# Optimization experiments

Measured on AMD Instinct MI355X. Metric: run time of the kernel, lower is better.

## Reference

```python
import jax, jax.numpy as jnp
import numpy as np

G = 16          # horizontal stripes
K = 4           # latents per stripe
TEMP = 0.125
TOPK_RATIO = 0.125
GATE_THR = 0.05
EPS = 1e-6
KSZ = 3


def setup_inputs() -> dict:
    key = jax.random.key(0)
    k1, k2 = jax.random.split(key)
    x = jax.random.normal(k1, (64, 256, 64, 44), dtype=jnp.float32)
    latent_basis = jax.random.normal(k2, (G, K, 256), dtype=jnp.float32)
    return {"x": x, "latent_basis": latent_basis}


def _avg_pool3(x):
    # x: [n, g, c, sh, w]; 3x3 avg pool, stride 1, pad 1, count_include_pad=True
    s = jax.lax.reduce_window(x, 0.0, jax.lax.add,
                              (1, 1, 1, KSZ, KSZ), (1, 1, 1, 1, 1),
                              [(0, 0), (0, 0), (0, 0), (1, 1), (1, 1)])
    return s / float(KSZ * KSZ)


def _l2norm(v, axis=-1):
    return v / jnp.maximum(jnp.linalg.norm(v, axis=axis, keepdims=True), 1e-12)


def reference(x, latent_basis):
    n, c, h, w = x.shape
    sh = h // G
    p = sh * w
    # split into horizontal stripes: [n, g, c, sh, w]
    xr = x.reshape(n, c, G, sh, w).transpose(0, 2, 1, 3, 4)
    support_feat = _avg_pool3(xr)
    feat_flat = xr.transpose(0, 1, 3, 4, 2).reshape(n, G, p, c)          # ngpc
    support_flat = support_feat.transpose(0, 1, 3, 4, 2).reshape(n, G, p, c)

    # active mask from detached feature energy
    e = jax.lax.stop_gradient(xr).astype(jnp.float32)
    fe = jnp.mean(e * e, axis=2)                                          # n g sh w
    fe = fe / jnp.maximum(jnp.max(fe, axis=(-2, -1), keepdims=True), EPS)
    active = (fe > GATE_THR).astype(jnp.float32)
    fallback = (fe > 0).astype(jnp.float32)
    use_fb = jnp.sum(active, axis=(-2, -1), keepdims=True) <= 0
    active = jnp.where(use_fb, fallback, active).reshape(n, G, p)

    # cosine-similarity routing
    sfn = _l2norm(support_flat)
    lbn = _l2norm(latent_basis)                                           # g k c
    logits = jnp.einsum('ngpc,gkc->ngpk', sfn, lbn) / TEMP
    route_prob = jax.nn.softmax(logits, axis=-1)
    support = route_prob * active[..., None]                              # n g p k
    pool_w = support / jnp.maximum(jnp.sum(support, axis=2, keepdims=True), EPS)
    tokens = jnp.einsum('ngpk,ngpc->ngkc', pool_w, feat_flat)
    tokens = tokens.transpose(0, 3, 1, 2).reshape(n, c, G * K)            # n c (g k)

    # top-k presence
    kk = max(1, min(p, int(p * TOPK_RATIO)))
    topv, _ = jax.lax.top_k(support.transpose(0, 1, 3, 2), kk)            # n g k kk
    presence = jnp.mean(topv, axis=-1).reshape(n, G * K)
    presence = presence / jnp.maximum(jnp.sum(presence, axis=1, keepdims=True), EPS)

    # scatter per-stripe maps back into full-resolution zero tensors
    eye = jnp.eye(G, dtype=support.dtype)
    loc_s = support.reshape(n, G, sh, w, K).transpose(0, 1, 4, 2, 3)      # n g k sh w
    loc_p = pool_w.reshape(n, G, sh, w, K).transpose(0, 1, 4, 2, 3)
    smap = jnp.einsum('ngksw,gG->ngkGsw', loc_s, eye).reshape(n, G * K, h, w)
    pmap = jnp.einsum('ngksw,gG->ngkGsw', loc_p, eye).reshape(n, G * K, h, w)
    support_flat_global = smap.transpose(0, 2, 3, 1).reshape(n, h * w, G * K)
    pool_weights_flat_global = pmap.transpose(0, 2, 3, 1).reshape(n, h * w, G * K)

    return (tokens.astype(x.dtype), presence.astype(x.dtype),
            support_flat_global.astype(x.dtype), pool_weights_flat_global.astype(x.dtype))
```

## Files before the change

kernel.cpp:

```cpp
#include <hip/hip_runtime.h>
#include <math.h>

#define GG   16
#define KK   4
#define NN   64
#define CC   256
#define SHH  4
#define WW   44
#define PP   176
#define HWSZ 2816
#define CHW  720896
#define TOPKK 22

template<int CTRL, int RMASK>
__device__ __forceinline__ float dpp0(float v) {
    return __int_as_float(__builtin_amdgcn_update_dpp(
        0, __float_as_int(v), CTRL, RMASK, 0xF, true));
}
__device__ __forceinline__ float nbrL(float v) { return dpp0<0x138, 0xF>(v); }
__device__ __forceinline__ float nbrR(float v) { return dpp0<0x130, 0xF>(v); }

__device__ __forceinline__ float wave_sum63(float v) {
    v += dpp0<0x111, 0xF>(v);
    v += dpp0<0x112, 0xF>(v);
    v += dpp0<0x114, 0xF>(v);
    v += dpp0<0x118, 0xF>(v);
    v += dpp0<0x142, 0xA>(v);
    v += dpp0<0x143, 0xC>(v);
    return v;
}
__device__ __forceinline__ float bcast63(float v) {
    return __int_as_float(__builtin_amdgcn_readlane(__float_as_int(v), 63));
}
__device__ __forceinline__ float wave_sum_all(float v) { return bcast63(wave_sum63(v)); }

__device__ __forceinline__ float wave_max_nn(float v) {
    v = fmaxf(v, dpp0<0x111, 0xF>(v));
    v = fmaxf(v, dpp0<0x112, 0xF>(v));
    v = fmaxf(v, dpp0<0x114, 0xF>(v));
    v = fmaxf(v, dpp0<0x118, 0xF>(v));
    v = fmaxf(v, dpp0<0x142, 0xA>(v));
    v = fmaxf(v, dpp0<0x143, 0xC>(v));
    return bcast63(v);
}

__global__ __launch_bounds__(512, 8) void routing_kernel(
    const float* __restrict__ x, const float* __restrict__ lb_raw,
    float* __restrict__ pres_ws,
    float4* __restrict__ outS, float4* __restrict__ outP,
    float* __restrict__ tok_out) {
    const int g = blockIdx.x;
    const int n = blockIdx.y;
    const int tid = threadIdx.x;
    const int w = __builtin_amdgcn_readfirstlane(tid >> 6);
    const int lane = tid & 63;
    const bool al = lane < WW;

    __shared__ float4 pd[8][PP];
    __shared__ float2 pnf[8][PP];
    __shared__ float4 lbn_lds[CC];
    __shared__ float redA[4], redB[4], zred[4][4];
    float4* sup4 = pd[2];
    float4* pw4  = pd[4];
    float4* pwT  = pd[6];

    if (w < 4) {
        const float* row = lb_raw + ((size_t)g * KK + w) * CC;
        float v0 = row[lane], v1 = row[lane + 64], v2 = row[lane + 128], v3 = row[lane + 192];
        float ss = v0 * v0 + v1 * v1 + v2 * v2 + v3 * v3;
        float tot = wave_sum_all(ss);
        float sc = (1.0f / 9.0f) / fmaxf(sqrtf(tot), 1e-12f);
        float* dst = (float*)lbn_lds;
        dst[lane * 4 + w]         = v0 * sc;
        dst[(lane + 64) * 4 + w]  = v1 * sc;
        dst[(lane + 128) * 4 + w] = v2 * sc;
        dst[(lane + 192) * 4 + w] = v3 * sc;
    }
    __syncthreads();

    const float* xb = x + (size_t)n * CHW + g * PP;
    const int c0 = w * 32;

    float4 dk[4];
    float nr[4] = {0, 0, 0, 0}, fe[4] = {0, 0, 0, 0};
    #pragma unroll
    for (int s = 0; s < 4; ++s) dk[s] = make_float4(0, 0, 0, 0);

    const float* xp = xb + (size_t)c0 * HWSZ + lane;
    float c0r = 0, c1r = 0, c2r = 0, c3r = 0;
    float n0r = 0, n1r = 0, n2r = 0, n3r = 0;
    if (al) {
        c0r = xp[0]; c1r = xp[44]; c2r = xp[88]; c3r = xp[132];
        n0r = xp[HWSZ]; n1r = xp[HWSZ + 44]; n2r = xp[HWSZ + 88]; n3r = xp[HWSZ + 132];
    }
    xp += 2 * HWSZ;
    #pragma unroll 1
    for (int i = 0; i < 32; ++i) {
        float f0 = 0, f1 = 0, f2 = 0, f3 = 0;
        if (i < 30 && al) { f0 = xp[0]; f1 = xp[44]; f2 = xp[88]; f3 = xp[132]; }
        xp += HWSZ;
        float4 lbv = lbn_lds[c0 + i];
        fe[0] += c0r * c0r; fe[1] += c1r * c1r; fe[2] += c2r * c2r; fe[3] += c3r * c3r;
        float h0 = c0r + nbrL(c0r) + nbrR(c0r);
        float h1 = c1r + nbrL(c1r) + nbrR(c1r);
        float h2 = c2r + nbrL(c2r) + nbrR(c2r);
        float h3 = c3r + nbrL(c3r) + nbrR(c3r);
        float p0 = h0 + h1;
        float p1 = p0 + h2;
        float t23 = h2 + h3;
        float p2 = h1 + t23;
        float p3 = t23;
        nr[0] += p0 * p0; nr[1] += p1 * p1; nr[2] += p2 * p2; nr[3] += p3 * p3;
        dk[0].x += p0 * lbv.x; dk[0].y += p0 * lbv.y; dk[0].z += p0 * lbv.z; dk[0].w += p0 * lbv.w;
        dk[1].x += p1 * lbv.x; dk[1].y += p1 * lbv.y; dk[1].z += p1 * lbv.z; dk[1].w += p1 * lbv.w;
        dk[2].x += p2 * lbv.x; dk[2].y += p2 * lbv.y; dk[2].z += p2 * lbv.z; dk[2].w += p2 * lbv.w;
        dk[3].x += p3 * lbv.x; dk[3].y += p3 * lbv.y; dk[3].z += p3 * lbv.z; dk[3].w += p3 * lbv.w;
        c0r = n0r; c1r = n1r; c2r = n2r; c3r = n3r;
        n0r = f0; n1r = f1; n2r = f2; n3r = f3;
    }
    if (al) {
        #pragma unroll
        for (int s = 0; s < 4; ++s) {
            pd[w][s * 44 + lane]  = dk[s];
            pnf[w][s * 44 + lane] = make_float2(nr[s], fe[s]);
        }
    }
    __syncthreads();

    if (tid < PP) {
        float4 a = pd[0][tid];
        #pragma unroll
        for (int ww = 1; ww < 8; ++ww) {
            float4 b = pd[ww][tid];
            a.x += b.x; a.y += b.y; a.z += b.z; a.w += b.w;
        }
        pd[0][tid] = a;
    } else if (tid >= 256 && tid < 256 + PP) {
        const int p = tid - 256;
        float2 a = pnf[0][p];
        #pragma unroll
        for (int ww = 1; ww < 8; ++ww) {
            float2 b = pnf[ww][p];
            a.x += b.x; a.y += b.y;
        }
        pnf[0][p] = a;
    }
    __syncthreads();

    const int s4 = w & 3;
    const int pix = s4 * 44 + (al ? lane : 0);
    float4 dv = pd[0][pix];
    float2 nf = pnf[0][pix];
    float nrm = nf.x;
    float fev = nf.y * (1.0f / 256.0f);

    float fmw = wave_max_nn(al ? fev : 0.0f);
    if (w < 4 && lane == 0) redA[s4] = fmw;
    __syncthreads();
    float femax = fmaxf(fmaxf(redA[0], redA[1]), fmaxf(redA[2], redA[3]));
    float den = fmaxf(femax, 1e-6f);
    bool pa = al && ((fev / den) > 0.05f);
    unsigned long long bl = __ballot((int)pa);
    if (w < 4 && lane == 0) redB[s4] = (float)__popcll(bl);
    __syncthreads();
    float cnt = redB[0] + redB[1] + redB[2] + redB[3];
    float actv = pa ? 1.0f : 0.0f;
    if (cnt <= 0.0f) actv = (al && (fev > 0.0f)) ? 1.0f : 0.0f;

    float inv = 72.0f / fmaxf(sqrtf(nrm), 9e-12f);
    float L0 = dv.x * inv, L1 = dv.y * inv, L2 = dv.z * inv, L3 = dv.w * inv;
    float mx = fmaxf(fmaxf(L0, L1), fmaxf(L2, L3));
    float e0 = expf(L0 - mx), e1 = expf(L1 - mx), e2 = expf(L2 - mx), e3 = expf(L3 - mx);
    float esum = e0 + e1 + e2 + e3;
    float sc = actv / esum;
    float s0 = e0 * sc, s1 = e1 * sc, s2 = e2 * sc, s3 = e3 * sc;

    float z0 = wave_sum63(s0), z1 = wave_sum63(s1), z2 = wave_sum63(s2), z3 = wave_sum63(s3);
    if (w < 4 && lane == 63) { zred[s4][0] = z0; zred[s4][1] = z1; zred[s4][2] = z2; zred[s4][3] = z3; }
    __syncthreads();
    float Z0 = zred[0][0] + zred[1][0] + zred[2][0] + zred[3][0];
    float Z1 = zred[0][1] + zred[1][1] + zred[2][1] + zred[3][1];
    float Z2 = zred[0][2] + zred[1][2] + zred[2][2] + zred[3][2];
    float Z3 = zred[0][3] + zred[1][3] + zred[2][3] + zred[3][3];
    float q0 = s0 / fmaxf(Z0, 1e-6f);
    float q1 = s1 / fmaxf(Z1, 1e-6f);
    float q2 = s2 / fmaxf(Z2, 1e-6f);
    float q3 = s3 / fmaxf(Z3, 1e-6f);

    if (w < 4 && al) {
        float4 qv = make_float4(q0, q1, q2, q3);
        sup4[pix] = make_float4(s0, s1, s2, s3);
        pw4[pix]  = qv;
        pwT[(pix & 3) * 44 + (pix >> 2)] = qv;
    }
    __syncthreads();

    if (w < 4) {
        const float* supf = (const float*)sup4;
        const int k = w;
        float v0 = supf[lane * 4 + k];
        float v1 = supf[(lane + 64) * 4 + k];
        float v2 = (lane < PP - 128) ? supf[(lane + 128) * 4 + k] : -1e30f;
        float tks = 0.0f;
        for (int it = 0; it < TOPKK; ++it) {
            float lm = fmaxf(v0, fmaxf(v1, v2));
            float M = wave_max_nn(lm);
            tks += M;
            unsigned long long mk = __ballot((int)(lm == M));
            int src = __ffsll(mk) - 1;
            if (lane == src) {
                if (v0 == M)      v0 = -1e30f;
                else if (v1 == M) v1 = -1e30f;
                else              v2 = -1e30f;
            }
        }
        if (lane == 0) pres_ws[(size_t)n * 64 + g * KK + k] = tks * (1.0f / (float)TOPKK);
    } else {
        const size_t obase = ((size_t)n * HWSZ + (size_t)g * PP) * 16;
        const float4 z = make_float4(0, 0, 0, 0);
        const int t0i = tid - 256;
        #pragma unroll 1
        for (int m = 0; m < 11; ++m) {
            const int j = t0i + m * 256;
            const int px = j >> 4, q = j & 15;
            const bool hit = (q == g);
            outS[obase + j] = hit ? sup4[px] : z;
            outP[obase + j] = hit ? pw4[px]  : z;
        }
    }

    {
        const bool a4 = lane < 44;
        float4 pwa = make_float4(0, 0, 0, 0), pwb = pwa, pwc = pwa, pwd = pwa;
        if (a4) {
            pwa = pwT[lane];
            pwb = pwT[44 + lane];
            pwc = pwT[88 + lane];
            pwd = pwT[132 + lane];
        }
        const float4* xq4 = (const float4*)(xb + (size_t)c0 * HWSZ) + lane;
        float4 tA = make_float4(0, 0, 0, 0), tB = tA, tC = tA;
        if (a4) { tA = xq4[0]; tB = xq4[704]; tC = xq4[1408]; }
        xq4 += 3 * 704;
        float* tokg = tok_out + ((size_t)n * CC + c0) * 64 + g * KK;

        #pragma unroll 1
        for (int i = 0; i < 32; ++i) {
            float4 tF = make_float4(0, 0, 0, 0);
            if (i < 29 && a4) tF = xq4[0];
            xq4 += 704;
            float t0 = tA.x * pwa.x + tA.y * pwb.x + tA.z * pwc.x + tA.w * pwd.x;
            float t1 = tA.x * pwa.y + tA.y * pwb.y + tA.z * pwc.y + tA.w * pwd.y;
            float t2 = tA.x * pwa.z + tA.y * pwb.z + tA.z * pwc.z + tA.w * pwd.z;
            float t3 = tA.x * pwa.w + tA.y * pwb.w + tA.z * pwc.w + tA.w * pwd.w;
            t0 = wave_sum63(t0); t1 = wave_sum63(t1); t2 = wave_sum63(t2); t3 = wave_sum63(t3);
            if (lane == 63) {
                *(float4*)(tokg + (size_t)i * 64) = make_float4(t0, t1, t2, t3);
            }
            tA = tB; tB = tC; tC = tF;
        }
    }
}

__global__ __launch_bounds__(64) void presence_kernel(
    const float* __restrict__ pres_ws, float* __restrict__ outp) {
    const int n = blockIdx.x;
    const int lane = threadIdx.x;
    float v = pres_ws[(size_t)n * 64 + lane];
    float tot = wave_sum_all(v);
    outp[(size_t)n * 64 + lane] = v / fmaxf(tot, 1e-6f);
}

extern "C" void kernel_launch(void* const* d_in, const int* in_sizes, int n_in,
                              void* d_out, int out_size, void* d_ws, size_t ws_size,
                              hipStream_t stream) {
    const float* x = (const float*)d_in[0];
    const float* lb = (const float*)d_in[1];
    float* ws = (float*)d_ws;
    float* pres_ws = ws;

    float* out = (float*)d_out;
    float* tok  = out;
    float* pres = out + 1048576;
    float* outS = out + 1052672;
    float* outP = outS + 11534336;

    routing_kernel<<<dim3(GG, NN), 512, 0, stream>>>(
        x, lb, pres_ws, (float4*)outS, (float4*)outP, tok);
    presence_kernel<<<NN, 64, 0, stream>>>(pres_ws, pres);
}
```

Baseline: 335.0 us.

## Load stripe pixels as float4 row-major and pool via bpermute neighbours

The first pass now loads each channel's stripe as contiguous float4 (4 consecutive pixels per lane) instead of four scalar row loads per lane. The horizontal neighbours come from in-register adds plus DPP across lanes with row-edge masks, and the vertical neighbours come from ds_bpermute. The prefetch is deepened to four channels in flight and the per-lane partials are transposed when written to LDS so they match the new pixel mapping. This aims to cut global load instruction count and improve coalescing, at the cost of LDS-path bpermute traffic.

```diff
diff --git a/kernel.cpp b/kernel.cpp
--- a/kernel.cpp
+++ b/kernel.cpp
@@ -43,6 +43,36 @@
     v = fmaxf(v, dpp0<0x143, 0xC>(v));
     return bcast63(v);
 }
+
+#define BPERM(a, x) __int_as_float(__builtin_amdgcn_ds_bpermute((a), __float_as_int(x)))
+
+#define POOL_STEP(VV, CH) do {                                                 \
+    const float4 lbv = lbn_lds[c0 + (CH)];                                     \
+    fe4.x += VV.x * VV.x; fe4.y += VV.y * VV.y;                                \
+    fe4.z += VV.z * VV.z; fe4.w += VV.w * VV.w;                                \
+    const float Lv = lmask * nbrL(VV.w);                                       \
+    const float Rv = rmask * nbrR(VV.x);                                       \
+    float4 h;                                                                  \
+    h.x = Lv + VV.x + VV.y;                                                    \
+    h.y = VV.x + VV.y + VV.z;                                                  \
+    h.z = VV.y + VV.z + VV.w;                                                  \
+    h.w = VV.z + VV.w + Rv;                                                    \
+    float4 p;                                                                  \
+    p.x = h.x + BPERM(addr_up, h.x) + BPERM(addr_dn, h.x);                     \
+    p.y = h.y + BPERM(addr_up, h.y) + BPERM(addr_dn, h.y);                     \
+    p.z = h.z + BPERM(addr_up, h.z) + BPERM(addr_dn, h.z);                     \
+    p.w = h.w + BPERM(addr_up, h.w) + BPERM(addr_dn, h.w);                     \
+    nr4.x += p.x * p.x; nr4.y += p.y * p.y;                                    \
+    nr4.z += p.z * p.z; nr4.w += p.w * p.w;                                    \
+    dk[0].x += p.x * lbv.x; dk[0].y += p.y * lbv.x;                            \
+    dk[0].z += p.z * lbv.x; dk[0].w += p.w * lbv.x;                            \
+    dk[1].x += p.x * lbv.y; dk[1].y += p.y * lbv.y;                            \
+    dk[1].z += p.z * lbv.y; dk[1].w += p.w * lbv.y;                            \
+    dk[2].x += p.x * lbv.z; dk[2].y += p.y * lbv.z;                            \
+    dk[2].z += p.z * lbv.z; dk[2].w += p.w * lbv.z;                            \
+    dk[3].x += p.x * lbv.w; dk[3].y += p.y * lbv.w;                            \
+    dk[3].z += p.z * lbv.w; dk[3].w += p.w * lbv.w;                            \
+} while (0)
 
 __global__ __launch_bounds__(512, 8) void routing_kernel(
     const float* __restrict__ x, const float* __restrict__ lb_raw,
@@ -81,49 +111,45 @@
     const float* xb = x + (size_t)n * CHW + g * PP;
     const int c0 = w * 32;
 
+    const int rr = lane / 11;
+    const int mm = lane - rr * 11;
+    const float lmask = (al && mm != 0)  ? 1.0f : 0.0f;
+    const float rmask = (al && mm != 10) ? 1.0f : 0.0f;
+    const int addr_up = ((lane < 11) ? (lane + 44) : (lane - 11)) * 4;
+    const int addr_dn = (lane + 11) * 4;
+
     float4 dk[4];
-    float nr[4] = {0, 0, 0, 0}, fe[4] = {0, 0, 0, 0};
     #pragma unroll
     for (int s = 0; s < 4; ++s) dk[s] = make_float4(0, 0, 0, 0);
-
-    const float* xp = xb + (size_t)c0 * HWSZ + lane;
-    float c0r = 0, c1r = 0, c2r = 0, c3r = 0;
-    float n0r = 0, n1r = 0, n2r = 0, n3r = 0;
+    float4 nr4 = make_float4(0, 0, 0, 0);
+    float4 fe4 = make_float4(0, 0, 0, 0);
+
+    const float4* xp4 = (const float4*)(xb + (size_t)c0 * HWSZ) + lane;
+    float4 sA = make_float4(0, 0, 0, 0), sB = sA, sC = sA, sD = sA;
+    if (al) { sA = xp4[0]; sB = xp4[704]; sC = xp4[1408]; sD = xp4[2112]; }
+
+    #pragma unroll 1
+    for (int i = 0; i < 32; i += 4) {
+        POOL_STEP(sA, i + 0);
+        if (i < 28 && al) sA = xp4[(size_t)(i + 4) * 704];
+        POOL_STEP(sB, i + 1);
+        if (i < 28 && al) sB = xp4[(size_t)(i + 5) * 704];
+        POOL_STEP(sC, i + 2);
+        if (i < 28 && al) sC = xp4[(size_t)(i + 6) * 704];
+        POOL_STEP(sD, i + 3);
+        if (i < 28 && al) sD = xp4[(size_t)(i + 7) * 704];
+    }
+
     if (al) {
-        c0r = xp[0]; c1r = xp[44]; c2r = xp[88]; c3r = xp[132];
-        n0r = xp[HWSZ]; n1r = xp[HWSZ + 44]; n2r = xp[HWSZ + 88]; n3r = xp[HWSZ + 132];
-    }
-    xp += 2 * HWSZ;
-    #pragma unroll 1
-    for (int i = 0; i < 32; ++i) {
-        float f0 = 0, f1 = 0, f2 = 0, f3 = 0;
-        if (i < 30 && al) { f0 = xp[0]; f1 = xp[44]; f2 = xp[88]; f3 = xp[132]; }
-        xp += HWSZ;
-        float4 lbv = lbn_lds[c0 + i];
-        fe[0] += c0r * c0r; fe[1] += c1r * c1r; fe[2] += c2r * c2r; fe[3] += c3r * c3r;
-        float h0 = c0r + nbrL(c0r) + nbrR(c0r);
-        float h1 = c1r + nbrL(c1r) + nbrR(c1r);
-        float h2 = c2r + nbrL(c2r) + nbrR(c2r);
-        float h3 = c3r + nbrL(c3r) + nbrR(c3r);
-        float p0 = h0 + h1;
-        float p1 = p0 + h2;
-        float t23 = h2 + h3;
-        float p2 = h1 + t23;
-        float p3 = t23;
-        nr[0] += p0 * p0; nr[1] += p1 * p1; nr[2] += p2 * p2; nr[3] += p3 * p3;
-        dk[0].x += p0 * lbv.x; dk[0].y += p0 * lbv.y; dk[0].z += p0 * lbv.z; dk[0].w += p0 * lbv.w;
-        dk[1].x += p1 * lbv.x; dk[1].y += p1 * lbv.y; dk[1].z += p1 * lbv.z; dk[1].w += p1 * lbv.w;
-        dk[2].x += p2 * lbv.x; dk[2].y += p2 * lbv.y; dk[2].z += p2 * lbv.z; dk[2].w += p2 * lbv.w;
-        dk[3].x += p3 * lbv.x; dk[3].y += p3 * lbv.y; dk[3].z += p3 * lbv.z; dk[3].w += p3 * lbv.w;
-        c0r = n0r; c1r = n1r; c2r = n2r; c3r = n3r;
-        n0r = f0; n1r = f1; n2r = f2; n3r = f3;
-    }
-    if (al) {
-        #pragma unroll
-        for (int s = 0; s < 4; ++s) {
-            pd[w][s * 44 + lane]  = dk[s];
-            pnf[w][s * 44 + lane] = make_float2(nr[s], fe[s]);
-        }
+        const int p0 = lane * 4;
+        pd[w][p0 + 0] = make_float4(dk[0].x, dk[1].x, dk[2].x, dk[3].x);
+        pd[w][p0 + 1] = make_float4(dk[0].y, dk[1].y, dk[2].y, dk[3].y);
+        pd[w][p0 + 2] = make_float4(dk[0].z, dk[1].z, dk[2].z, dk[3].z);
+        pd[w][p0 + 3] = make_float4(dk[0].w, dk[1].w, dk[2].w, dk[3].w);
+        pnf[w][p0 + 0] = make_float2(nr4.x, fe4.x);
+        pnf[w][p0 + 1] = make_float2(nr4.y, fe4.y);
+        pnf[w][p0 + 2] = make_float2(nr4.z, fe4.z);
+        pnf[w][p0 + 3] = make_float2(nr4.w, fe4.w);
     }
     __syncthreads();
 
@@ -230,9 +256,8 @@
     }
 
     {
-        const bool a4 = lane < 44;
         float4 pwa = make_float4(0, 0, 0, 0), pwb = pwa, pwc = pwa, pwd = pwa;
-        if (a4) {
+        if (al) {
             pwa = pwT[lane];
             pwb = pwT[44 + lane];
             pwc = pwT[88 + lane];
@@ -240,14 +265,14 @@
         }
         const float4* xq4 = (const float4*)(xb + (size_t)c0 * HWSZ) + lane;
         float4 tA = make_float4(0, 0, 0, 0), tB = tA, tC = tA;
-        if (a4) { tA = xq4[0]; tB = xq4[704]; tC = xq4[1408]; }
+        if (al) { tA = xq4[0]; tB = xq4[704]; tC = xq4[1408]; }
         xq4 += 3 * 704;
         float* tokg = tok_out + ((size_t)n * CC + c0) * 64 + g * KK;
 
         #pragma unroll 1
         for (int i = 0; i < 32; ++i) {
             float4 tF = make_float4(0, 0, 0, 0);
-            if (i < 29 && a4) tF = xq4[0];
+            if (i < 29 && al) tF = xq4[0];
             xq4 += 704;
             float t0 = tA.x * pwa.x + tA.y * pwb.x + tA.z * pwc.x + tA.w * pwd.x;
             float t1 = tA.x * pwa.y + tA.y * pwb.y + tA.z * pwc.y + tA.w * pwd.y;
```

After: 765.5 us. 129% more time.
